# Kernel optimization log

Measured on AMD Instinct MI355X. Metric: run time of the kernel, lower is better.

Reference implementation:

```python
import jax, jax.numpy as jnp
import numpy as np

N = 50000      # nodes
E = 800000     # edges
IN_DIM = 128
HID = 16       # per-head hidden dim (layer1)
HEADS = 8
OUT_DIM = 32   # layer2 output dim (1 head)
NEG_SLOPE = 0.2  # GAT-paper LeakyReLU slope


def _gat_layer(x, W, a_src, a_dst, src, dst, num_nodes):
    """One multi-head GAT layer.
    x: [N, Fin]; W: [Fin, H*D]; a_src/a_dst: [H, D]; src/dst: [E].
    Returns [N, H, D].
    """
    H, D = a_src.shape
    z = (x @ W).reshape(num_nodes, H, D)            # [N, H, D]
    # edge attention logits: attn_fc([z_src || z_dst]) split into two dots
    e_s = jnp.einsum('nhd,hd->nh', z, a_src)        # [N, H]
    e_d = jnp.einsum('nhd,hd->nh', z, a_dst)        # [N, H]
    e = e_s[src] + e_d[dst]                          # [E, H]
    e = jnp.where(e >= 0, e, NEG_SLOPE * e)          # leaky_relu
    # softmax over incoming edges of each destination node
    m = jax.ops.segment_max(e, dst, num_segments=num_nodes)   # [N, H]
    ex = jnp.exp(e - m[dst])                                   # [E, H]
    s = jax.ops.segment_sum(ex, dst, num_segments=num_nodes)  # [N, H]
    alpha = ex / s[dst]                                        # [E, H]
    msg = alpha[:, :, None] * z[src]                            # [E, H, D]
    return jax.ops.segment_sum(msg, dst, num_segments=num_nodes)  # [N, H, D]


def setup_inputs() -> dict:
    key = jax.random.key(0)
    ks = jax.random.split(key, 9)
    h = jax.random.normal(ks[0], (N, IN_DIM), dtype=jnp.float32)
    src = jax.random.randint(ks[1], (E,), 0, N, dtype=jnp.int32)
    dst = jax.random.randint(ks[2], (E,), 0, N, dtype=jnp.int32)
    sc1 = 1.0 / np.sqrt(IN_DIM)
    W1 = jax.random.normal(ks[3], (IN_DIM, HEADS * HID), dtype=jnp.float32) * sc1
    a1_src = jax.random.normal(ks[4], (HEADS, HID), dtype=jnp.float32) * 0.1
    a1_dst = jax.random.normal(ks[5], (HEADS, HID), dtype=jnp.float32) * 0.1
    sc2 = 1.0 / np.sqrt(HEADS * HID)
    W2 = jax.random.normal(ks[6], (HEADS * HID, OUT_DIM), dtype=jnp.float32) * sc2
    a2_src = jax.random.normal(ks[7], (1, OUT_DIM), dtype=jnp.float32) * 0.1
    a2_dst = jax.random.normal(ks[8], (1, OUT_DIM), dtype=jnp.float32) * 0.1
    return {"h": h, "W1": W1, "a1_src": a1_src, "a1_dst": a1_dst,
            "W2": W2, "a2_src": a2_src, "a2_dst": a2_dst,
            "src": src, "dst": dst}


def reference(h, W1, a1_src, a1_dst, W2, a2_src, a2_dst, src, dst):
    # layer1: multi-head, concat heads -> [N, HEADS*HID]
    h1 = _gat_layer(h, W1, a1_src, a1_dst, src, dst, N).reshape(N, HEADS * HID)
    h1 = jax.nn.elu(h1)
    # layer2: single head -> [N, OUT_DIM]
    out = _gat_layer(h1, W2, a2_src, a2_dst, src, dst, N).reshape(N, OUT_DIM)
    return out
```

## Files before the change

### kernel.cpp

```cpp
#include <hip/hip_runtime.h>
#include <hip/hip_fp16.h>
#include <math.h>

#define NN 50000
#define EE 800000
#define FIN 128
#define F1  128
#define NH  8
#define DH  16
#define F2  32
#define SLOPE 0.2f
#define LOG2E 1.44269504f

#define EB 4096
#define NBLK ((EE + EB - 1) / EB)
#define BK  391
#define SEGCAP 4096
#define PREPB 80
#define GEMM1B ((NN + 63) / 64)
#define ATT1B  (((NN + 127) / 128) * 8)
#define GEMM2B ((NN + 63) / 64)

typedef _Float16 f16x8 __attribute__((ext_vector_type(8)));
typedef float    f32x4 __attribute__((ext_vector_type(4)));

__global__ __launch_bounds__(256) void k1_hist_prep(const int* __restrict__ dst,
        const float* __restrict__ W1, const float* __restrict__ W2,
        __half* __restrict__ wt1, __half* __restrict__ wt2, int* __restrict__ hist) {
    int tid = threadIdx.x;
    if (blockIdx.x < NBLK) {
        __shared__ int lc[BK];
        for (int i = tid; i < BK; i += 256) lc[i] = 0;
        __syncthreads();
        int base = blockIdx.x * EB;
        int end = base + EB; if (end > EE) end = EE;
        for (int i = base + tid; i < end; i += 256)
            atomicAdd(&lc[dst[i] >> 7], 1);
        __syncthreads();
        for (int i = tid; i < BK; i += 256)
            if (lc[i]) atomicAdd(&hist[i], lc[i]);
    } else {
        int gidx = (blockIdx.x - NBLK) * 256 + tid;
        if (gidx < FIN * F1) {
            int n = gidx >> 7, k = gidx & 127;
            wt1[gidx] = __float2half(W1[k * F1 + n]);
        } else {
            int t2 = gidx - FIN * F1;
            if (t2 < F2 * FIN) {
                int n = t2 >> 7, k = t2 & 127;
                wt2[t2] = __float2half(W2[k * F2 + n]);
            }
        }
    }
}

extern __shared__ char smem_k2[];
__global__ __launch_bounds__(256) void k2_split_gemm1(const int* __restrict__ src,
        const int* __restrict__ dst, const int* __restrict__ hist, int* __restrict__ cursor,
        unsigned int* __restrict__ sorted,
        const float* __restrict__ h, const __half* __restrict__ wt1,
        const float* __restrict__ a1s, const float* __restrict__ a1d,
        __half* __restrict__ z1s, float* __restrict__ es1s, float* __restrict__ ed1s) {
    int tid = threadIdx.x;
    if (blockIdx.x < NBLK) {
        unsigned int*   recs = (unsigned int*)smem_k2;
        unsigned short* rbk  = (unsigned short*)(smem_k2 + 16384);
        int* lc    = (int*)(smem_k2 + 24576);
        int* lofs  = (int*)(smem_k2 + 26624);
        int* lcur  = (int*)(smem_k2 + 28672);
        int* delta = (int*)(smem_k2 + 30720);
        int* bscan = (int*)(smem_k2 + 32768);
        int* sh    = (int*)(smem_k2 + 34816);
        for (int i = tid; i < 512; i += 256) lc[i] = 0;
        __syncthreads();
        int base = blockIdx.x * EB;
        int cnt = EE - base; if (cnt > EB) cnt = EB;
        unsigned int myrec[16];
        #pragma unroll
        for (int k = 0; k < 16; ++k) {
            int i = base + tid + k * 256;
            myrec[k] = 0xFFFFFFFFu;
            if (i - base < cnt) {
                unsigned int d = (unsigned int)dst[i];
                myrec[k] = (d << 16) | (unsigned int)src[i];
                atomicAdd(&lc[d >> 7], 1);
            }
        }
        __syncthreads();
        int a0 = lc[2 * tid], a1 = lc[2 * tid + 1];
        int tsum = a0 + a1;
        sh[tid] = tsum;
        __syncthreads();
        for (int off = 1; off < 256; off <<= 1) {
            int t = (tid >= off) ? sh[tid - off] : 0;
            __syncthreads(); sh[tid] += t; __syncthreads();
        }
        int ex = sh[tid] - tsum;
        lofs[2 * tid] = ex;
        lofs[2 * tid + 1] = ex + a0;
        __syncthreads();
        int h0 = hist[2 * tid], h1 = hist[2 * tid + 1];
        int hsum = h0 + h1;
        sh[tid] = hsum;
        __syncthreads();
        for (int off = 1; off < 256; off <<= 1) {
            int t = (tid >= off) ? sh[tid - off] : 0;
            __syncthreads(); sh[tid] += t; __syncthreads();
        }
        int hex = sh[tid] - hsum;
        bscan[2 * tid] = hex;
        bscan[2 * tid + 1] = hex + h0;
        __syncthreads();
        for (int b = tid; b < BK; b += 256) {
            int c = lc[b];
            lcur[b] = lofs[b];
            if (c) {
                int g = atomicAdd(&cursor[b], c);
                delta[b] = bscan[b] + g - lofs[b];
            }
        }
        __syncthreads();
        #pragma unroll
        for (int k = 0; k < 16; ++k) {
            if (myrec[k] != 0xFFFFFFFFu) {
                int b = (int)(myrec[k] >> 23);
                int pos = atomicAdd(&lcur[b], 1);
                recs[pos] = myrec[k];
                rbk[pos] = (unsigned short)b;
            }
        }
        __syncthreads();
        for (int s = tid; s < cnt; s += 256)
            sorted[s + delta[rbk[s]]] = recs[s];
    } else {
        __half* hs  = (__half*)smem_k2;
        __half* wls = (__half*)(smem_k2 + 17408);
        for (int c = tid; c < 2048; c += 256) {
            int row = c >> 4, ch = c & 15;
            *(float4*)&wls[row * 136 + ch * 8] = *(const float4*)&wt1[row * 128 + ch * 8];
        }
        int rowBase = (blockIdx.x - NBLK) * 64;
        for (int idx4 = tid; idx4 < 64 * 32; idx4 += 256) {
            int r = idx4 >> 5, cc = (idx4 & 31) * 4;
            int n = rowBase + r;
            float4 v = (n < NN) ? *(const float4*)&h[(size_t)n * FIN + cc] : make_float4(0, 0, 0, 0);
            union { __half2 h2[2]; int2 i; } u;
            u.h2[0] = __floats2half2_rn(v.x, v.y);
            u.h2[1] = __floats2half2_rn(v.z, v.w);
            *(int2*)&hs[r * 136 + cc] = u.i;
        }
        __syncthreads();
        int l = tid & 63, w = tid >> 6;
        int q = l >> 4, cl = l & 15;
        int m0 = w * 16;
        float as[8], ad[8];
        #pragma unroll
        for (int t = 0; t < 8; ++t) { as[t] = a1s[t * DH + cl]; ad[t] = a1d[t * DH + cl]; }
        f32x4 acc[8];
        #pragma unroll
        for (int t = 0; t < 8; ++t) acc[t] = (f32x4){0.f, 0.f, 0.f, 0.f};
        const __half* ap = &hs[(m0 + cl) * 136 + q * 8];
        const __half* bp = &wls[cl * 136 + q * 8];
        #pragma unroll
        for (int k0 = 0; k0 < 128; k0 += 32) {
            f16x8 af = *(const f16x8*)(ap + k0);
            #pragma unroll
            for (int t = 0; t < 8; ++t) {
                f16x8 bf = *(const f16x8*)(bp + t * 16 * 136 + k0);
                acc[t] = __builtin_amdgcn_mfma_f32_16x16x32_f16(af, bf, acc[t], 0, 0, 0);
            }
        }
        #pragma unroll
        for (int t = 0; t < 8; ++t) {
            #pragma unroll
            for (int reg = 0; reg < 4; ++reg) {
                int row = rowBase + m0 + q * 4 + reg;
                float z = acc[t][reg];
                float s = z * as[t], d = z * ad[t];
                s += __shfl_xor(s, 1, 64); d += __shfl_xor(d, 1, 64);
                s += __shfl_xor(s, 2, 64); d += __shfl_xor(d, 2, 64);
                s += __shfl_xor(s, 4, 64); d += __shfl_xor(d, 4, 64);
                s += __shfl_xor(s, 8, 64); d += __shfl_xor(d, 8, 64);
                if (row < NN) {
                    z1s[(size_t)t * (NN * 16) + (size_t)row * 16 + cl] = __float2half(z);
                    if (cl == 0) {
                        es1s[(size_t)t * NN + row] = s * LOG2E;
                        ed1s[(size_t)t * NN + row] = d * LOG2E;
                    }
                }
            }
        }
    }
}

__global__ __launch_bounds__(256) void csrbuild_kernel(const int* __restrict__ hist,
        const unsigned int* __restrict__ sorted, unsigned short* __restrict__ csr,
        int* __restrict__ row_ptr) {
    __shared__ unsigned int recs[SEGCAP];
    __shared__ unsigned short csr_sh[SEGCAP];
    __shared__ int ncnt[128], ncur[128];
    __shared__ int sh[256];
    __shared__ int bscan[512];
    int b = blockIdx.x;
    int tid = threadIdx.x;
    int h0 = hist[2 * tid], h1 = hist[2 * tid + 1];
    int hsum = h0 + h1;
    sh[tid] = hsum;
    if (tid < 128) ncnt[tid] = 0;
    __syncthreads();
    for (int off = 1; off < 256; off <<= 1) {
        int t = (tid >= off) ? sh[tid - off] : 0;
        __syncthreads(); sh[tid] += t; __syncthreads();
    }
    int hex = sh[tid] - hsum;
    bscan[2 * tid] = hex;
    bscan[2 * tid + 1] = hex + h0;
    __syncthreads();
    int s0 = bscan[b], s1 = bscan[b + 1];
    int cnt = s1 - s0; if (cnt > SEGCAP) cnt = SEGCAP;
    for (int i = tid; i < cnt; i += 256) {
        unsigned int r = sorted[s0 + i];
        recs[i] = r;
        atomicAdd(&ncnt[(r >> 16) & 127], 1);
    }
    __syncthreads();
    int v = (tid < 128) ? ncnt[tid] : 0;
    sh[tid] = v;
    __syncthreads();
    for (int off = 1; off < 256; off <<= 1) {
        int t = (tid >= off) ? sh[tid - off] : 0;
        __syncthreads(); sh[tid] += t; __syncthreads();
    }
    int ex = sh[tid] - v;
    if (tid < 128) {
        ncur[tid] = ex;
        int node = b * 128 + tid;
        if (node < NN) row_ptr[node] = s0 + ex;
    }
    if (b == BK - 1 && tid == 0) row_ptr[NN] = EE;
    __syncthreads();
    for (int i = tid; i < cnt; i += 256) {
        unsigned int r = recs[i];
        int local = (r >> 16) & 127;
        int p = atomicAdd(&ncur[local], 1);
        csr_sh[p] = (unsigned short)(r & 0xFFFFu);
    }
    __syncthreads();
    for (int i = tid; i < cnt; i += 256)
        csr[s0 + i] = csr_sh[i];
}

__global__ __launch_bounds__(256) void attn1_slice_kernel(const int* __restrict__ row_ptr,
        const unsigned short* __restrict__ csr, const __half* __restrict__ z1s,
        const float* __restrict__ es, const float* __restrict__ ed,
        __half* __restrict__ h1s) {
    int hl = blockIdx.x & 7;
    int n = (blockIdx.x >> 3) * 128 + (threadIdx.x >> 1);
    if (n >= NN) return;
    int j = threadIdx.x & 1;
    const __half* zp = z1s + (size_t)hl * (NN * 16) + j * 8;
    const float* esp = es + (size_t)hl * NN;
    int b0 = row_ptr[n];
    int cnt = row_ptr[n + 1] - b0;
    float edn = ed[(size_t)hl * NN + n];
    float acc[8] = {0.f, 0.f, 0.f, 0.f, 0.f, 0.f, 0.f, 0.f};
    float ws = 0.f;
    int i = 0;
    for (; i + 4 <= cnt; i += 4) {
        int s0 = csr[b0 + i], s1 = csr[b0 + i + 1], s2 = csr[b0 + i + 2], s3 = csr[b0 + i + 3];
        float e0 = esp[s0] + edn;
        float e1 = esp[s1] + edn;
        float e2 = esp[s2] + edn;
        float e3 = esp[s3] + edn;
        union { float4 f; __half2 h2[4]; } u0, u1, u2, u3;
        u0.f = *(const float4*)&zp[(size_t)s0 * 16];
        u1.f = *(const float4*)&zp[(size_t)s1 * 16];
        u2.f = *(const float4*)&zp[(size_t)s2 * 16];
        u3.f = *(const float4*)&zp[(size_t)s3 * 16];
        float w0 = exp2f(e0 >= 0.f ? e0 : SLOPE * e0);
        float w1 = exp2f(e1 >= 0.f ? e1 : SLOPE * e1);
        float w2 = exp2f(e2 >= 0.f ? e2 : SLOPE * e2);
        float w3 = exp2f(e3 >= 0.f ? e3 : SLOPE * e3);
        ws += (w0 + w1) + (w2 + w3);
        #pragma unroll
        for (int t = 0; t < 4; ++t) {
            float2 v0 = __half22float2(u0.h2[t]);
            float2 v1 = __half22float2(u1.h2[t]);
            float2 v2 = __half22float2(u2.h2[t]);
            float2 v3 = __half22float2(u3.h2[t]);
            acc[2*t]   = fmaf(w0, v0.x, fmaf(w1, v1.x, fmaf(w2, v2.x, fmaf(w3, v3.x, acc[2*t]))));
            acc[2*t+1] = fmaf(w0, v0.y, fmaf(w1, v1.y, fmaf(w2, v2.y, fmaf(w3, v3.y, acc[2*t+1]))));
        }
    }
    for (; i < cnt; ++i) {
        int s = csr[b0 + i];
        float e = esp[s] + edn;
        float wv = exp2f(e >= 0.f ? e : SLOPE * e);
        ws += wv;
        union { float4 f; __half2 h2[4]; } u;
        u.f = *(const float4*)&zp[(size_t)s * 16];
        #pragma unroll
        for (int t = 0; t < 4; ++t) {
            float2 v = __half22float2(u.h2[t]);
            acc[2*t]   = fmaf(wv, v.x, acc[2*t]);
            acc[2*t+1] = fmaf(wv, v.y, acc[2*t+1]);
        }
    }
    float rs = ws > 0.f ? 1.0f / ws : 0.f;
    union { float4 f; __half2 h2[4]; } p;
    #pragma unroll
    for (int t = 0; t < 4; ++t) {
        float x0 = acc[2*t] * rs, x1 = acc[2*t+1] * rs;
        x0 = x0 > 0.f ? x0 : __expf(x0) - 1.0f;
        x1 = x1 > 0.f ? x1 : __expf(x1) - 1.0f;
        p.h2[t] = __floats2half2_rn(x0, x1);
    }
    *(float4*)&h1s[(size_t)hl * (NN * 16) + (size_t)n * 16 + j * 8] = p.f;
}

__global__ __launch_bounds__(256) void gemm2_kernel(const __half* __restrict__ h1s,
        const __half* __restrict__ wt2, const float* __restrict__ a2s, const float* __restrict__ a2d,
        __half* __restrict__ z2h, float* __restrict__ es2x, float* __restrict__ ed2x) {
    __shared__ alignas(16) __half hs[64 * 136];
    __shared__ alignas(16) __half wls[32 * 136];
    int tid = threadIdx.x;
    for (int c = tid; c < 512; c += 256) {
        int row = c >> 4, ch = c & 15;
        *(float4*)&wls[row * 136 + ch * 8] = *(const float4*)&wt2[row * 128 + ch * 8];
    }
    int rowBase = blockIdx.x * 64;
    for (int idx = tid; idx < 1024; idx += 256) {
        int j2 = idx & 1, nl = (idx >> 1) & 63, pl = idx >> 7;
        int n = rowBase + nl;
        float4 v = (n < NN) ? *(const float4*)&h1s[(size_t)pl * (NN * 16) + (size_t)n * 16 + j2 * 8]
                            : make_float4(0, 0, 0, 0);
        *(float4*)&hs[nl * 136 + pl * 16 + j2 * 8] = v;
    }
    __syncthreads();
    int l = tid & 63, w = tid >> 6;
    int q = l >> 4, cl = l & 15;
    int m0 = w * 16;
    float as0 = a2s[cl], as1 = a2s[16 + cl];
    float ad0 = a2d[cl], ad1 = a2d[16 + cl];
    f32x4 acc2[2];
    acc2[0] = (f32x4){0.f, 0.f, 0.f, 0.f};
    acc2[1] = (f32x4){0.f, 0.f, 0.f, 0.f};
    const __half* ap = &hs[(m0 + cl) * 136 + q * 8];
    const __half* bp = &wls[cl * 136 + q * 8];
    #pragma unroll
    for (int k0 = 0; k0 < 128; k0 += 32) {
        f16x8 af = *(const f16x8*)(ap + k0);
        #pragma unroll
        for (int t = 0; t < 2; ++t) {
            f16x8 bf = *(const f16x8*)(bp + t * 16 * 136 + k0);
            acc2[t] = __builtin_amdgcn_mfma_f32_16x16x32_f16(af, bf, acc2[t], 0, 0, 0);
        }
    }
    #pragma unroll
    for (int reg = 0; reg < 4; ++reg) {
        int row = rowBase + m0 + q * 4 + reg;
        float s = acc2[0][reg] * as0 + acc2[1][reg] * as1;
        float d = acc2[0][reg] * ad0 + acc2[1][reg] * ad1;
        s += __shfl_xor(s, 1, 64); d += __shfl_xor(d, 1, 64);
        s += __shfl_xor(s, 2, 64); d += __shfl_xor(d, 2, 64);
        s += __shfl_xor(s, 4, 64); d += __shfl_xor(d, 4, 64);
        s += __shfl_xor(s, 8, 64); d += __shfl_xor(d, 8, 64);
        if (row < NN) {
            z2h[(size_t)row * F2 + cl]      = __float2half(acc2[0][reg]);
            z2h[(size_t)row * F2 + 16 + cl] = __float2half(acc2[1][reg]);
            if (cl == 0) {
                es2x[row] = s * LOG2E;
                ed2x[row] = d * LOG2E;
            }
        }
    }
}

__global__ __launch_bounds__(256) void attn2_kernel(const int* __restrict__ row_ptr,
        const unsigned short* __restrict__ csr, const __half* __restrict__ z2h,
        const float* __restrict__ es, const float* __restrict__ ed,
        float* __restrict__ out) {
    int gt = blockIdx.x * 256 + threadIdx.x;
    int n = gt >> 3;
    int j = gt & 7;
    if (n >= NN) return;
    int b0 = row_ptr[n];
    int cnt = row_ptr[n + 1] - b0;
    float edn = ed[n];
    float acc[4] = {0.f, 0.f, 0.f, 0.f};
    float ws = 0.f;
    int i = 0;
    for (; i + 4 <= cnt; i += 4) {
        int s0 = csr[b0 + i], s1 = csr[b0 + i + 1], s2 = csr[b0 + i + 2], s3 = csr[b0 + i + 3];
        float e0 = es[s0] + edn;
        float e1 = es[s1] + edn;
        float e2 = es[s2] + edn;
        float e3 = es[s3] + edn;
        union { float2 f; __half2 h2[2]; } u0, u1, u2, u3;
        u0.f = *(const float2*)&z2h[(size_t)s0 * F2 + j * 4];
        u1.f = *(const float2*)&z2h[(size_t)s1 * F2 + j * 4];
        u2.f = *(const float2*)&z2h[(size_t)s2 * F2 + j * 4];
        u3.f = *(const float2*)&z2h[(size_t)s3 * F2 + j * 4];
        float w0 = exp2f(e0 >= 0.f ? e0 : SLOPE * e0);
        float w1 = exp2f(e1 >= 0.f ? e1 : SLOPE * e1);
        float w2 = exp2f(e2 >= 0.f ? e2 : SLOPE * e2);
        float w3 = exp2f(e3 >= 0.f ? e3 : SLOPE * e3);
        ws += (w0 + w1) + (w2 + w3);
        #pragma unroll
        for (int t = 0; t < 2; ++t) {
            float2 v0 = __half22float2(u0.h2[t]);
            float2 v1 = __half22float2(u1.h2[t]);
            float2 v2 = __half22float2(u2.h2[t]);
            float2 v3 = __half22float2(u3.h2[t]);
            acc[2*t]   = fmaf(w0, v0.x, fmaf(w1, v1.x, fmaf(w2, v2.x, fmaf(w3, v3.x, acc[2*t]))));
            acc[2*t+1] = fmaf(w0, v0.y, fmaf(w1, v1.y, fmaf(w2, v2.y, fmaf(w3, v3.y, acc[2*t+1]))));
        }
    }
    for (; i < cnt; ++i) {
        int s = csr[b0 + i];
        float e = es[s] + edn;
        float wv = exp2f(e >= 0.f ? e : SLOPE * e);
        ws += wv;
        union { float2 f; __half2 h2[2]; } u;
        u.f = *(const float2*)&z2h[(size_t)s * F2 + j * 4];
        #pragma unroll
        for (int t = 0; t < 2; ++t) {
            float2 v = __half22float2(u.h2[t]);
            acc[2*t]   = fmaf(wv, v.x, acc[2*t]);
            acc[2*t+1] = fmaf(wv, v.y, acc[2*t+1]);
        }
    }
    float rs = ws > 0.f ? 1.0f / ws : 0.f;
    *(float4*)&out[(size_t)n * F2 + j * 4] =
        make_float4(acc[0]*rs, acc[1]*rs, acc[2]*rs, acc[3]*rs);
}

extern "C" void kernel_launch(void* const* d_in, const int* in_sizes, int n_in,
                              void* d_out, int out_size, void* d_ws, size_t ws_size,
                              hipStream_t stream) {
    const float* h   = (const float*)d_in[0];
    const float* W1  = (const float*)d_in[1];
    const float* a1s = (const float*)d_in[2];
    const float* a1d = (const float*)d_in[3];
    const float* W2  = (const float*)d_in[4];
    const float* a2s = (const float*)d_in[5];
    const float* a2d = (const float*)d_in[6];
    const int*   src = (const int*)d_in[7];
    const int*   dst = (const int*)d_in[8];
    float* out = (float*)d_out;

    int* ip      = (int*)d_ws;
    int* hist    = ip;
    int* cursor  = hist + 512;
    int* row_ptr = cursor + 512;
    unsigned int* sorted = (unsigned int*)(row_ptr + NN + 8);
    unsigned short* csr16 = (unsigned short*)(sorted + EE);
    float* es1s = (float*)(csr16 + EE);
    float* ed1s = es1s + (size_t)NN * NH;
    float* es2x = ed1s + (size_t)NN * NH;
    float* ed2x = es2x + NN;
    __half* z1s = (__half*)(ed2x + NN);
    __half* z2h = z1s + (size_t)NN * F1;
    __half* wt1 = z2h + (size_t)NN * F2;
    __half* wt2 = wt1 + FIN * F1;
    __half* h1s = wt2 + F2 * FIN;

    hipMemsetAsync(hist, 0, 1024 * sizeof(int), stream);

    k1_hist_prep<<<NBLK + PREPB, 256, 0, stream>>>(dst, W1, W2, wt1, wt2, hist);
    k2_split_gemm1<<<NBLK + GEMM1B, 256, 52224, stream>>>(src, dst, hist, cursor, sorted,
                                                          h, wt1, a1s, a1d, z1s, es1s, ed1s);
    csrbuild_kernel<<<BK, 256, 0, stream>>>(hist, sorted, csr16, row_ptr);
    attn1_slice_kernel<<<ATT1B, 256, 0, stream>>>(row_ptr, csr16, z1s, es1s, ed1s, h1s);
    gemm2_kernel<<<GEMM2B, 256, 0, stream>>>(h1s, wt2, a2s, a2d, z2h, es2x, ed2x);
    attn2_kernel<<<(NN * 8 + 255) / 256, 256, 0, stream>>>(row_ptr, csr16, z2h, es2x, ed2x, out);
}
```

Before: 210.5 us.

## Precompute per-edge attention weights once in CSR build and a new w2 kernel

Moves the LeakyReLU+exp2 edge-weight computation out of the aggregation kernels. Layer 1 weights for all 8 heads are computed once per edge in csrbuild, where the source node's logits are read as node-major float4s and the destination logits come from shared memory. Layer 2 weights come from a new w2_kernel that uses a stored per-edge local destination byte. Previously each aggregation thread recomputed exp per edge, with j-duplicated threads and scattered es lookups. The trade is an extra 32 B/edge write and read of precomputed weights, plus one extra launch.

```diff
diff --git a/kernel.cpp b/kernel.cpp
--- a/kernel.cpp
+++ b/kernel.cpp
@@ -60,7 +60,7 @@
         unsigned int* __restrict__ sorted,
         const float* __restrict__ h, const __half* __restrict__ wt1,
         const float* __restrict__ a1s, const float* __restrict__ a1d,
-        __half* __restrict__ z1s, float* __restrict__ es1s, float* __restrict__ ed1s) {
+        __half* __restrict__ z1s, float* __restrict__ es1x, float* __restrict__ ed1x) {
     int tid = threadIdx.x;
     if (blockIdx.x < NBLK) {
         unsigned int*   recs = (unsigned int*)smem_k2;
@@ -184,8 +184,8 @@
                 if (row < NN) {
                     z1s[(size_t)t * (NN * 16) + (size_t)row * 16 + cl] = __float2half(z);
                     if (cl == 0) {
-                        es1s[(size_t)t * NN + row] = s * LOG2E;
-                        ed1s[(size_t)t * NN + row] = d * LOG2E;
+                        es1x[row * NH + t] = s * LOG2E;
+                        ed1x[row * NH + t] = d * LOG2E;
                     }
                 }
             }
@@ -195,9 +195,13 @@
 
 __global__ __launch_bounds__(256) void csrbuild_kernel(const int* __restrict__ hist,
         const unsigned int* __restrict__ sorted, unsigned short* __restrict__ csr,
-        int* __restrict__ row_ptr) {
+        unsigned char* __restrict__ dstl,
+        const float* __restrict__ es1x, const float* __restrict__ ed1x,
+        float* __restrict__ w1p, int* __restrict__ row_ptr) {
     __shared__ unsigned int recs[SEGCAP];
     __shared__ unsigned short csr_sh[SEGCAP];
+    __shared__ unsigned char dst_sh[SEGCAP];
+    __shared__ float ed_sh[128 * NH];
     __shared__ int ncnt[128], ncur[128];
     __shared__ int sh[256];
     __shared__ int bscan[512];
@@ -207,6 +211,10 @@
     int hsum = h0 + h1;
     sh[tid] = hsum;
     if (tid < 128) ncnt[tid] = 0;
+    for (int idx = tid; idx < 128 * NH; idx += 256) {
+        int node = b * 128 + (idx >> 3);
+        ed_sh[idx] = (node < NN) ? ed1x[node * NH + (idx & 7)] : 0.f;
+    }
     __syncthreads();
     for (int off = 1; off < 256; off <<= 1) {
         int t = (tid >= off) ? sh[tid - off] : 0;
@@ -244,43 +252,49 @@
         int local = (r >> 16) & 127;
         int p = atomicAdd(&ncur[local], 1);
         csr_sh[p] = (unsigned short)(r & 0xFFFFu);
-    }
-    __syncthreads();
-    for (int i = tid; i < cnt; i += 256)
-        csr[s0 + i] = csr_sh[i];
+        dst_sh[p] = (unsigned char)local;
+    }
+    __syncthreads();
+    for (int i = tid; i < cnt; i += 256) {
+        unsigned short sv = csr_sh[i];
+        unsigned char lv = dst_sh[i];
+        csr[s0 + i] = sv;
+        dstl[s0 + i] = lv;
+        float4 ea = *(const float4*)&es1x[(size_t)sv * NH];
+        float4 eb = *(const float4*)&es1x[(size_t)sv * NH + 4];
+        float es8[8] = {ea.x, ea.y, ea.z, ea.w, eb.x, eb.y, eb.z, eb.w};
+        const float* edp = &ed_sh[(int)lv * NH];
+        #pragma unroll
+        for (int hh = 0; hh < 8; ++hh) {
+            float e = es8[hh] + edp[hh];
+            e = e >= 0.f ? e : SLOPE * e;
+            w1p[(size_t)hh * EE + s0 + i] = exp2f(e);
+        }
+    }
 }
 
 __global__ __launch_bounds__(256) void attn1_slice_kernel(const int* __restrict__ row_ptr,
         const unsigned short* __restrict__ csr, const __half* __restrict__ z1s,
-        const float* __restrict__ es, const float* __restrict__ ed,
-        __half* __restrict__ h1s) {
+        const float* __restrict__ w1p, __half* __restrict__ h1s) {
     int hl = blockIdx.x & 7;
     int n = (blockIdx.x >> 3) * 128 + (threadIdx.x >> 1);
     if (n >= NN) return;
     int j = threadIdx.x & 1;
     const __half* zp = z1s + (size_t)hl * (NN * 16) + j * 8;
-    const float* esp = es + (size_t)hl * NN;
+    const float* wp = w1p + (size_t)hl * EE;
     int b0 = row_ptr[n];
     int cnt = row_ptr[n + 1] - b0;
-    float edn = ed[(size_t)hl * NN + n];
     float acc[8] = {0.f, 0.f, 0.f, 0.f, 0.f, 0.f, 0.f, 0.f};
     float ws = 0.f;
     int i = 0;
     for (; i + 4 <= cnt; i += 4) {
         int s0 = csr[b0 + i], s1 = csr[b0 + i + 1], s2 = csr[b0 + i + 2], s3 = csr[b0 + i + 3];
-        float e0 = esp[s0] + edn;
-        float e1 = esp[s1] + edn;
-        float e2 = esp[s2] + edn;
-        float e3 = esp[s3] + edn;
+        float w0 = wp[b0 + i], w1 = wp[b0 + i + 1], w2 = wp[b0 + i + 2], w3 = wp[b0 + i + 3];
         union { float4 f; __half2 h2[4]; } u0, u1, u2, u3;
         u0.f = *(const float4*)&zp[(size_t)s0 * 16];
         u1.f = *(const float4*)&zp[(size_t)s1 * 16];
         u2.f = *(const float4*)&zp[(size_t)s2 * 16];
         u3.f = *(const float4*)&zp[(size_t)s3 * 16];
-        float w0 = exp2f(e0 >= 0.f ? e0 : SLOPE * e0);
-        float w1 = exp2f(e1 >= 0.f ? e1 : SLOPE * e1);
-        float w2 = exp2f(e2 >= 0.f ? e2 : SLOPE * e2);
-        float w3 = exp2f(e3 >= 0.f ? e3 : SLOPE * e3);
         ws += (w0 + w1) + (w2 + w3);
         #pragma unroll
         for (int t = 0; t < 4; ++t) {
@@ -294,8 +308,7 @@
     }
     for (; i < cnt; ++i) {
         int s = csr[b0 + i];
-        float e = esp[s] + edn;
-        float wv = exp2f(e >= 0.f ? e : SLOPE * e);
+        float wv = wp[b0 + i];
         ws += wv;
         union { float4 f; __half2 h2[4]; } u;
         u.f = *(const float4*)&zp[(size_t)s * 16];
@@ -376,35 +389,43 @@
     }
 }
 
+__global__ __launch_bounds__(256) void w2_kernel(const int* __restrict__ row_ptr,
+        const unsigned short* __restrict__ csr, const unsigned char* __restrict__ dstl,
+        const float* __restrict__ es2x, const float* __restrict__ ed2x,
+        float* __restrict__ w2p) {
+    int b = blockIdx.x;
+    int s0 = row_ptr[b * 128];
+    int nend = (b + 1) * 128; if (nend > NN) nend = NN;
+    int s1 = row_ptr[nend];
+    for (int i = s0 + threadIdx.x; i < s1; i += 256) {
+        int s = csr[i];
+        int n = b * 128 + (int)dstl[i];
+        float e = es2x[s] + ed2x[n];
+        e = e >= 0.f ? e : SLOPE * e;
+        w2p[i] = exp2f(e);
+    }
+}
+
 __global__ __launch_bounds__(256) void attn2_kernel(const int* __restrict__ row_ptr,
         const unsigned short* __restrict__ csr, const __half* __restrict__ z2h,
-        const float* __restrict__ es, const float* __restrict__ ed,
-        float* __restrict__ out) {
+        const float* __restrict__ w2p, float* __restrict__ out) {
     int gt = blockIdx.x * 256 + threadIdx.x;
     int n = gt >> 3;
     int j = gt & 7;
     if (n >= NN) return;
     int b0 = row_ptr[n];
     int cnt = row_ptr[n + 1] - b0;
-    float edn = ed[n];
     float acc[4] = {0.f, 0.f, 0.f, 0.f};
     float ws = 0.f;
     int i = 0;
     for (; i + 4 <= cnt; i += 4) {
         int s0 = csr[b0 + i], s1 = csr[b0 + i + 1], s2 = csr[b0 + i + 2], s3 = csr[b0 + i + 3];
-        float e0 = es[s0] + edn;
-        float e1 = es[s1] + edn;
-        float e2 = es[s2] + edn;
-        float e3 = es[s3] + edn;
+        float w0 = w2p[b0 + i], w1 = w2p[b0 + i + 1], w2 = w2p[b0 + i + 2], w3 = w2p[b0 + i + 3];
         union { float2 f; __half2 h2[2]; } u0, u1, u2, u3;
         u0.f = *(const float2*)&z2h[(size_t)s0 * F2 + j * 4];
         u1.f = *(const float2*)&z2h[(size_t)s1 * F2 + j * 4];
         u2.f = *(const float2*)&z2h[(size_t)s2 * F2 + j * 4];
         u3.f = *(const float2*)&z2h[(size_t)s3 * F2 + j * 4];
-        float w0 = exp2f(e0 >= 0.f ? e0 : SLOPE * e0);
-        float w1 = exp2f(e1 >= 0.f ? e1 : SLOPE * e1);
-        float w2 = exp2f(e2 >= 0.f ? e2 : SLOPE * e2);
-        float w3 = exp2f(e3 >= 0.f ? e3 : SLOPE * e3);
         ws += (w0 + w1) + (w2 + w3);
         #pragma unroll
         for (int t = 0; t < 2; ++t) {
@@ -418,8 +439,7 @@
     }
     for (; i < cnt; ++i) {
         int s = csr[b0 + i];
-        float e = es[s] + edn;
-        float wv = exp2f(e >= 0.f ? e : SLOPE * e);
+        float wv = w2p[b0 + i];
         ws += wv;
         union { float2 f; __half2 h2[2]; } u;
         u.f = *(const float2*)&z2h[(size_t)s * F2 + j * 4];
@@ -455,23 +475,27 @@
     int* row_ptr = cursor + 512;
     unsigned int* sorted = (unsigned int*)(row_ptr + NN + 8);
     unsigned short* csr16 = (unsigned short*)(sorted + EE);
-    float* es1s = (float*)(csr16 + EE);
-    float* ed1s = es1s + (size_t)NN * NH;
-    float* es2x = ed1s + (size_t)NN * NH;
+    unsigned char* dstl = (unsigned char*)(csr16 + EE);
+    float* es1x = (float*)(dstl + EE);
+    float* ed1x = es1x + (size_t)NN * NH;
+    float* es2x = ed1x + (size_t)NN * NH;
     float* ed2x = es2x + NN;
     __half* z1s = (__half*)(ed2x + NN);
     __half* z2h = z1s + (size_t)NN * F1;
     __half* wt1 = z2h + (size_t)NN * F2;
     __half* wt2 = wt1 + FIN * F1;
     __half* h1s = wt2 + F2 * FIN;
+    float* w1p  = (float*)(h1s + (size_t)NN * F1);
+    float* w2p  = (float*)sorted;
 
     hipMemsetAsync(hist, 0, 1024 * sizeof(int), stream);
 
     k1_hist_prep<<<NBLK + PREPB, 256, 0, stream>>>(dst, W1, W2, wt1, wt2, hist);
     k2_split_gemm1<<<NBLK + GEMM1B, 256, 52224, stream>>>(src, dst, hist, cursor, sorted,
-                                                          h, wt1, a1s, a1d, z1s, es1s, ed1s);
-    csrbuild_kernel<<<BK, 256, 0, stream>>>(hist, sorted, csr16, row_ptr);
-    attn1_slice_kernel<<<ATT1B, 256, 0, stream>>>(row_ptr, csr16, z1s, es1s, ed1s, h1s);
+                                                          h, wt1, a1s, a1d, z1s, es1x, ed1x);
+    csrbuild_kernel<<<BK, 256, 0, stream>>>(hist, sorted, csr16, dstl, es1x, ed1x, w1p, row_ptr);
+    attn1_slice_kernel<<<ATT1B, 256, 0, stream>>>(row_ptr, csr16, z1s, w1p, h1s);
     gemm2_kernel<<<GEMM2B, 256, 0, stream>>>(h1s, wt2, a2s, a2d, z2h, es2x, ed2x);
-    attn2_kernel<<<(NN * 8 + 255) / 256, 256, 0, stream>>>(row_ptr, csr16, z2h, es2x, ed2x, out);
-}
+    w2_kernel<<<BK, 256, 0, stream>>>(row_ptr, csr16, dstl, es2x, ed2x, w2p);
+    attn2_kernel<<<(NN * 8 + 255) / 256, 256, 0, stream>>>(row_ptr, csr16, z2h, w2p, out);
+}
```

Result: no change. 212.1 us (+0.7%).
